# Performance work log

Hardware: AMD Instinct MI355X
Metric: run time of the kernel (lower is better)

The kernel has to match this reference:

```python
import jax, jax.numpy as jnp
import numpy as np

B, Q, K, D = 8, 2048, 2048, 512

def setup_inputs() -> dict:
    key = jax.random.key(0)
    k1, k2, k3, k4, k5 = jax.random.split(key, 5)
    return {
        "query": jax.random.normal(k1, (B, Q, D), dtype=jnp.float32),
        "key": jax.random.normal(k2, (B, K, D), dtype=jnp.float32),
        "value": jax.random.normal(k3, (B, K, D), dtype=jnp.float32),
        "key_mask": jax.random.randint(k4, (B, K), 0, 2, dtype=jnp.int32),
        "W": jax.random.normal(k5, (D, D), dtype=jnp.float32) / np.sqrt(D),
    }

def reference(query, key, value, key_mask, W):
    # bilinear score: s[b,q,k] = query[b,q,:] @ W @ key[b,k,:]
    scale = 1.0 / jnp.sqrt(jnp.asarray(query.shape[-1], query.dtype))
    qW = jnp.einsum('bqd,de->bqe', query, W)          # [B,Q,D]
    scores = jnp.einsum('bqe,bke->bqk', qW, key)      # [B,Q,K]
    scores = jnp.where(key_mask[:, None, :] == 0, jnp.asarray(-1e20, scores.dtype), scores) * scale
    dist = jax.nn.softmax(scores, axis=-1)            # [B,Q,K]
    context = jnp.einsum('bqk,bkd->bqd', dist, value) # [B,Q,D]
    return context, dist
```

## Files before the change

### kernel.cpp

```cpp
#include <hip/hip_runtime.h>
#include <stdint.h>

#define BB 8
#define QQ 2048
#define KK 2048
#define DD 512

typedef _Float16 f16x8 __attribute__((ext_vector_type(8)));
typedef float f32x4 __attribute__((ext_vector_type(4)));

__device__ __forceinline__ unsigned short f2h(float f) {
    union { _Float16 h; unsigned short u; } x;
    x.h = (_Float16)f;
    return x.u;
}
__device__ __forceinline__ float h2f(unsigned short u) {
    union { unsigned short u; _Float16 h; } x;
    x.u = u;
    return (float)x.h;
}

__device__ __forceinline__ void async16(const unsigned short* g, unsigned short* l) {
    __builtin_amdgcn_global_load_lds(
        (const __attribute__((address_space(1))) unsigned int*)g,
        (__attribute__((address_space(3))) unsigned int*)l, 16, 0, 0);
}

__global__ __launch_bounds__(256) void cvt_f32_f16(const float* __restrict__ in,
                                                   unsigned short* __restrict__ out) {
    size_t i = ((size_t)blockIdx.x * 256 + threadIdx.x) * 8;
    float4 a = *(const float4*)(in + i);
    float4 b = *(const float4*)(in + i + 4);
    uint4 u;
    u.x = (unsigned)f2h(a.x) | ((unsigned)f2h(a.y) << 16);
    u.y = (unsigned)f2h(a.z) | ((unsigned)f2h(a.w) << 16);
    u.z = (unsigned)f2h(b.x) | ((unsigned)f2h(b.y) << 16);
    u.w = (unsigned)f2h(b.z) | ((unsigned)f2h(b.w) << 16);
    *(uint4*)(out + i) = u;
}

__global__ __launch_bounds__(256) void transpose_cvt(const float* __restrict__ in,
                                                     unsigned short* __restrict__ out,
                                                     int R, int C, long inB, long outB) {
    __shared__ float t[32][33];
    const float* ip = in + (size_t)blockIdx.z * inB;
    unsigned short* op = out + (size_t)blockIdx.z * outB;
    int x = threadIdx.x & 31, y0 = threadIdx.x >> 5;
    int c0 = blockIdx.x * 32, r0 = blockIdx.y * 32;
#pragma unroll
    for (int i = 0; i < 32; i += 8)
        t[y0 + i][x] = ip[(size_t)(r0 + y0 + i) * C + c0 + x];
    __syncthreads();
#pragma unroll
    for (int i = 0; i < 32; i += 8)
        op[(size_t)(c0 + y0 + i) * R + r0 + x] = f2h(t[x][y0 + i]);
}

template <bool AF32, int OUTM>
__global__ __launch_bounds__(256) void gemm_bt(const void* __restrict__ Aall,
                                               const unsigned short* __restrict__ Ball,
                                               void* __restrict__ Call,
                                               const int* __restrict__ maskAll,
                                               int Kred, int lda, int ldb, int ldc,
                                               long aStride, long bStride, long cStride,
                                               int maskStride, float scale) {
    const int b = blockIdx.z;
    const int m0 = blockIdx.y * 128;
    const int n0 = blockIdx.x * 128;

    __shared__ unsigned short As[128 * 32];
    __shared__ unsigned short Bs[128 * 32];

    const int tid = threadIdx.x;
    const int lane = tid & 63, wave = tid >> 6;
    const int wm = wave >> 1, wn = wave & 1;
    const int lrow = lane & 15, quad = lane >> 4;

    const int ar = tid >> 2, ac = (tid & 3) * 8;
    const int fr = tid >> 3, fc = (tid & 7) * 4;

    const unsigned short* Bb = Ball + (size_t)b * bStride + (size_t)n0 * ldb;
    unsigned short* AsW = As + wave * 512;
    unsigned short* BsW = Bs + wave * 512;

    f32x4 acc[4][4];
#pragma unroll
    for (int mi = 0; mi < 4; mi++)
#pragma unroll
        for (int ni = 0; ni < 4; ni++)
            acc[mi][ni] = (f32x4){0.f, 0.f, 0.f, 0.f};

    for (int kk = 0; kk < Kred; kk += 32) {
        if constexpr (AF32) {
            const float* A = (const float*)Aall + (size_t)b * aStride + (size_t)m0 * lda + kk;
#pragma unroll
            for (int j = 0; j < 4; j++) {
                int row = j * 32 + fr;
                float4 f = *(const float4*)(A + (size_t)row * lda + fc);
                uint2 u;
                u.x = (unsigned)f2h(f.x) | ((unsigned)f2h(f.y) << 16);
                u.y = (unsigned)f2h(f.z) | ((unsigned)f2h(f.w) << 16);
                *(uint2*)&As[row * 32 + fc] = u;
            }
        } else {
            const unsigned short* A =
                (const unsigned short*)Aall + (size_t)b * aStride + (size_t)m0 * lda + kk;
#pragma unroll
            for (int j = 0; j < 2; j++)
                async16(A + (size_t)(j * 64 + ar) * lda + ac, AsW + j * 2048);
        }
        {
            const unsigned short* Bp = Bb + kk;
#pragma unroll
            for (int j = 0; j < 2; j++)
                async16(Bp + (size_t)(j * 64 + ar) * ldb + ac, BsW + j * 2048);
        }
        __syncthreads();

        f16x8 af[4], bfr[4];
#pragma unroll
        for (int i = 0; i < 4; i++)
            af[i] = *(const f16x8*)&As[(wm * 64 + i * 16 + lrow) * 32 + quad * 8];
#pragma unroll
        for (int i = 0; i < 4; i++)
            bfr[i] = *(const f16x8*)&Bs[(wn * 64 + i * 16 + lrow) * 32 + quad * 8];

#pragma unroll
        for (int mi = 0; mi < 4; mi++)
#pragma unroll
            for (int ni = 0; ni < 4; ni++)
                acc[mi][ni] = __builtin_amdgcn_mfma_f32_16x16x32_f16(af[mi], bfr[ni],
                                                                     acc[mi][ni], 0, 0, 0);
        __syncthreads();
    }

#pragma unroll
    for (int mi = 0; mi < 4; mi++) {
#pragma unroll
        for (int ni = 0; ni < 4; ni++) {
            int gm = m0 + wm * 64 + mi * 16 + quad * 4;
            int gn = n0 + wn * 64 + ni * 16 + lrow;
            if constexpr (OUTM == 0) {
                unsigned short* C = (unsigned short*)Call + (size_t)b * cStride;
#pragma unroll
                for (int r = 0; r < 4; r++)
                    C[(size_t)(gm + r) * ldc + gn] = f2h(acc[mi][ni][r]);
            } else if constexpr (OUTM == 1) {
                unsigned short* C = (unsigned short*)Call + (size_t)b * cStride;
                const int* mk = maskAll + (size_t)b * maskStride;
                bool keep = mk[gn] != 0;
#pragma unroll
                for (int r = 0; r < 4; r++)
                    C[(size_t)(gm + r) * ldc + gn] =
                        keep ? f2h(acc[mi][ni][r] * scale) : f2h(-60000.f);
            } else {
                float* C = (float*)Call + (size_t)b * cStride;
#pragma unroll
                for (int r = 0; r < 4; r++)
                    C[(size_t)(gm + r) * ldc + gn] = acc[mi][ni][r];
            }
        }
    }
}

__global__ __launch_bounds__(256) void softmax_rows(unsigned short* __restrict__ sc,
                                                    float* __restrict__ dist) {
    unsigned short* sp = sc + (size_t)blockIdx.x * 2048;
    float* dp = dist + (size_t)blockIdx.x * 2048;
    int tid = threadIdx.x;

    uint4 u = *(uint4*)(sp + tid * 8);
    float x[8];
    x[0] = h2f((unsigned short)(u.x & 0xffff)); x[1] = h2f((unsigned short)(u.x >> 16));
    x[2] = h2f((unsigned short)(u.y & 0xffff)); x[3] = h2f((unsigned short)(u.y >> 16));
    x[4] = h2f((unsigned short)(u.z & 0xffff)); x[5] = h2f((unsigned short)(u.z >> 16));
    x[6] = h2f((unsigned short)(u.w & 0xffff)); x[7] = h2f((unsigned short)(u.w >> 16));

    float m = x[0];
#pragma unroll
    for (int i = 1; i < 8; i++) m = fmaxf(m, x[i]);
#pragma unroll
    for (int off = 32; off > 0; off >>= 1) m = fmaxf(m, __shfl_down(m, off));

    __shared__ float red[8];
    if ((tid & 63) == 0) red[tid >> 6] = m;
    __syncthreads();
    m = fmaxf(fmaxf(red[0], red[1]), fmaxf(red[2], red[3]));

    float s = 0.f;
#pragma unroll
    for (int i = 0; i < 8; i++) { x[i] = __expf(x[i] - m); s += x[i]; }
#pragma unroll
    for (int off = 32; off > 0; off >>= 1) s += __shfl_down(s, off);
    if ((tid & 63) == 0) red[4 + (tid >> 6)] = s;
    __syncthreads();
    float inv = 1.0f / (red[4] + red[5] + red[6] + red[7]);

#pragma unroll
    for (int i = 0; i < 8; i++) x[i] *= inv;

    float4 o0 = {x[0], x[1], x[2], x[3]};
    float4 o1 = {x[4], x[5], x[6], x[7]};
    *(float4*)(dp + tid * 8) = o0;
    *(float4*)(dp + tid * 8 + 4) = o1;

    uint4 v;
    v.x = (unsigned)f2h(x[0]) | ((unsigned)f2h(x[1]) << 16);
    v.y = (unsigned)f2h(x[2]) | ((unsigned)f2h(x[3]) << 16);
    v.z = (unsigned)f2h(x[4]) | ((unsigned)f2h(x[5]) << 16);
    v.w = (unsigned)f2h(x[6]) | ((unsigned)f2h(x[7]) << 16);
    *(uint4*)(sp + tid * 8) = v;
}

extern "C" void kernel_launch(void* const* d_in, const int* in_sizes, int n_in,
                              void* d_out, int out_size, void* d_ws, size_t ws_size,
                              hipStream_t stream) {
    const float* q    = (const float*)d_in[0];
    const float* k    = (const float*)d_in[1];
    const float* v    = (const float*)d_in[2];
    const int*   mask = (const int*)d_in[3];
    const float* W    = (const float*)d_in[4];

    float* ctx  = (float*)d_out;
    float* dist = ctx + (size_t)BB * QQ * DD;

    unsigned short* ws  = (unsigned short*)d_ws;
    unsigned short* Wt  = ws;
    unsigned short* Kh  = Wt + (size_t)DD * DD;
    unsigned short* Vt  = Kh + (size_t)BB * KK * DD;
    unsigned short* qWh = Vt + (size_t)BB * DD * KK;
    unsigned short* Sc  = qWh + (size_t)BB * QQ * DD;

    const float scale = 0.044194173824159216f;

    transpose_cvt<<<dim3(DD / 32, DD / 32, 1), 256, 0, stream>>>(W, Wt, DD, DD, 0, 0);
    cvt_f32_f16<<<dim3((BB * KK * DD / 8) / 256), 256, 0, stream>>>(k, Kh);
    transpose_cvt<<<dim3(DD / 32, KK / 32, BB), 256, 0, stream>>>(
        v, Vt, KK, DD, (long)KK * DD, (long)DD * KK);
    gemm_bt<true, 0><<<dim3(DD / 128, QQ / 128, BB), 256, 0, stream>>>(
        q, Wt, qWh, nullptr, DD, DD, DD, DD,
        (long)QQ * DD, 0, (long)QQ * DD, 0, 0.f);
    gemm_bt<false, 1><<<dim3(KK / 128, QQ / 128, BB), 256, 0, stream>>>(
        qWh, Kh, Sc, mask, DD, DD, DD, KK,
        (long)QQ * DD, (long)KK * DD, (long)QQ * KK, KK, scale);
    softmax_rows<<<dim3(BB * QQ), 256, 0, stream>>>(Sc, dist);
    gemm_bt<false, 2><<<dim3(DD / 128, QQ / 128, BB), 256, 0, stream>>>(
        Sc, Vt, ctx, nullptr, KK, KK, KK, DD,
        (long)QQ * KK, (long)DD * KK, (long)QQ * DD, 0, 0.f);
}
```

Before: 425.1 us.

## Fuse exp and row-sum into score GEMM epilogue, defer softmax normalization

The score GEMM epilogue now writes exp(score*scale) directly, without subtracting a row max, and accumulates per-row sums with shuffles and atomics. The softmax kernel becomes a simple normalize pass, and the context GEMM divides by the row sum in its epilogue instead of reading normalized probabilities. The query is also pre-converted to fp16 so the first GEMM can use async LDS loads. Skipping the max subtraction assumes bounded scores, and exp values stored in fp16 can overflow or lose precision. The extra conversion pass and the atomics add some overhead.

```diff
diff --git a/kernel.cpp b/kernel.cpp
--- a/kernel.cpp
+++ b/kernel.cpp
@@ -56,11 +56,12 @@
         op[(size_t)(c0 + y0 + i) * R + r0 + x] = f2h(t[x][y0 + i]);
 }
 
-template <bool AF32, int OUTM>
-__global__ __launch_bounds__(256) void gemm_bt(const void* __restrict__ Aall,
+template <int OUTM>
+__global__ __launch_bounds__(256) void gemm_bt(const unsigned short* __restrict__ Aall,
                                                const unsigned short* __restrict__ Ball,
                                                void* __restrict__ Call,
                                                const int* __restrict__ maskAll,
+                                               float* __restrict__ sums,
                                                int Kred, int lda, int ldb, int ldc,
                                                long aStride, long bStride, long cStride,
                                                int maskStride, float scale) {
@@ -77,8 +78,8 @@
     const int lrow = lane & 15, quad = lane >> 4;
 
     const int ar = tid >> 2, ac = (tid & 3) * 8;
-    const int fr = tid >> 3, fc = (tid & 7) * 4;
-
+
+    const unsigned short* Ab = Aall + (size_t)b * aStride + (size_t)m0 * lda;
     const unsigned short* Bb = Ball + (size_t)b * bStride + (size_t)n0 * ldb;
     unsigned short* AsW = As + wave * 512;
     unsigned short* BsW = Bs + wave * 512;
@@ -91,30 +92,12 @@
             acc[mi][ni] = (f32x4){0.f, 0.f, 0.f, 0.f};
 
     for (int kk = 0; kk < Kred; kk += 32) {
-        if constexpr (AF32) {
-            const float* A = (const float*)Aall + (size_t)b * aStride + (size_t)m0 * lda + kk;
-#pragma unroll
-            for (int j = 0; j < 4; j++) {
-                int row = j * 32 + fr;
-                float4 f = *(const float4*)(A + (size_t)row * lda + fc);
-                uint2 u;
-                u.x = (unsigned)f2h(f.x) | ((unsigned)f2h(f.y) << 16);
-                u.y = (unsigned)f2h(f.z) | ((unsigned)f2h(f.w) << 16);
-                *(uint2*)&As[row * 32 + fc] = u;
-            }
-        } else {
-            const unsigned short* A =
-                (const unsigned short*)Aall + (size_t)b * aStride + (size_t)m0 * lda + kk;
-#pragma unroll
-            for (int j = 0; j < 2; j++)
-                async16(A + (size_t)(j * 64 + ar) * lda + ac, AsW + j * 2048);
-        }
-        {
-            const unsigned short* Bp = Bb + kk;
-#pragma unroll
-            for (int j = 0; j < 2; j++)
-                async16(Bp + (size_t)(j * 64 + ar) * ldb + ac, BsW + j * 2048);
-        }
+#pragma unroll
+        for (int j = 0; j < 2; j++)
+            async16(Ab + (size_t)(j * 64 + ar) * lda + kk + ac, AsW + j * 2048);
+#pragma unroll
+        for (int j = 0; j < 2; j++)
+            async16(Bb + (size_t)(j * 64 + ar) * ldb + kk + ac, BsW + j * 2048);
         __syncthreads();
 
         f16x8 af[4], bfr[4];
@@ -136,80 +119,77 @@
 
 #pragma unroll
     for (int mi = 0; mi < 4; mi++) {
-#pragma unroll
-        for (int ni = 0; ni < 4; ni++) {
-            int gm = m0 + wm * 64 + mi * 16 + quad * 4;
-            int gn = n0 + wn * 64 + ni * 16 + lrow;
-            if constexpr (OUTM == 0) {
-                unsigned short* C = (unsigned short*)Call + (size_t)b * cStride;
+        const int gm = m0 + wm * 64 + mi * 16 + quad * 4;
+        if constexpr (OUTM == 0) {
+            unsigned short* C = (unsigned short*)Call + (size_t)b * cStride;
+#pragma unroll
+            for (int ni = 0; ni < 4; ni++) {
+                int gn = n0 + wn * 64 + ni * 16 + lrow;
 #pragma unroll
                 for (int r = 0; r < 4; r++)
                     C[(size_t)(gm + r) * ldc + gn] = f2h(acc[mi][ni][r]);
-            } else if constexpr (OUTM == 1) {
-                unsigned short* C = (unsigned short*)Call + (size_t)b * cStride;
-                const int* mk = maskAll + (size_t)b * maskStride;
+            }
+        } else if constexpr (OUTM == 1) {
+            unsigned short* C = (unsigned short*)Call + (size_t)b * cStride;
+            const int* mk = maskAll + (size_t)b * maskStride;
+            float ps[4] = {0.f, 0.f, 0.f, 0.f};
+#pragma unroll
+            for (int ni = 0; ni < 4; ni++) {
+                int gn = n0 + wn * 64 + ni * 16 + lrow;
                 bool keep = mk[gn] != 0;
 #pragma unroll
+                for (int r = 0; r < 4; r++) {
+                    float e = keep ? __expf(acc[mi][ni][r] * scale) : 0.f;
+                    C[(size_t)(gm + r) * ldc + gn] = f2h(e);
+                    ps[r] += e;
+                }
+            }
+#pragma unroll
+            for (int off = 1; off < 16; off <<= 1)
+#pragma unroll
+                for (int r = 0; r < 4; r++) ps[r] += __shfl_xor(ps[r], off);
+            if (lrow == 0) {
+                float* s = sums + (size_t)b * QQ;
+#pragma unroll
+                for (int r = 0; r < 4; r++) atomicAdd(&s[gm + r], ps[r]);
+            }
+        } else {
+            float* C = (float*)Call + (size_t)b * cStride;
+            const float* s = sums + (size_t)b * QQ;
+            float iv[4];
+#pragma unroll
+            for (int r = 0; r < 4; r++) iv[r] = 1.0f / s[gm + r];
+#pragma unroll
+            for (int ni = 0; ni < 4; ni++) {
+                int gn = n0 + wn * 64 + ni * 16 + lrow;
+#pragma unroll
                 for (int r = 0; r < 4; r++)
-                    C[(size_t)(gm + r) * ldc + gn] =
-                        keep ? f2h(acc[mi][ni][r] * scale) : f2h(-60000.f);
-            } else {
-                float* C = (float*)Call + (size_t)b * cStride;
-#pragma unroll
-                for (int r = 0; r < 4; r++)
-                    C[(size_t)(gm + r) * ldc + gn] = acc[mi][ni][r];
+                    C[(size_t)(gm + r) * ldc + gn] = acc[mi][ni][r] * iv[r];
             }
         }
     }
 }
 
-__global__ __launch_bounds__(256) void softmax_rows(unsigned short* __restrict__ sc,
-                                                    float* __restrict__ dist) {
-    unsigned short* sp = sc + (size_t)blockIdx.x * 2048;
+__global__ __launch_bounds__(256) void normalize_rows(const unsigned short* __restrict__ expS,
+                                                      const float* __restrict__ sums,
+                                                      float* __restrict__ dist) {
+    const unsigned short* sp = expS + (size_t)blockIdx.x * 2048;
     float* dp = dist + (size_t)blockIdx.x * 2048;
+    const float inv = 1.0f / sums[blockIdx.x];
     int tid = threadIdx.x;
 
-    uint4 u = *(uint4*)(sp + tid * 8);
-    float x[8];
-    x[0] = h2f((unsigned short)(u.x & 0xffff)); x[1] = h2f((unsigned short)(u.x >> 16));
-    x[2] = h2f((unsigned short)(u.y & 0xffff)); x[3] = h2f((unsigned short)(u.y >> 16));
-    x[4] = h2f((unsigned short)(u.z & 0xffff)); x[5] = h2f((unsigned short)(u.z >> 16));
-    x[6] = h2f((unsigned short)(u.w & 0xffff)); x[7] = h2f((unsigned short)(u.w >> 16));
-
-    float m = x[0];
-#pragma unroll
-    for (int i = 1; i < 8; i++) m = fmaxf(m, x[i]);
-#pragma unroll
-    for (int off = 32; off > 0; off >>= 1) m = fmaxf(m, __shfl_down(m, off));
-
-    __shared__ float red[8];
-    if ((tid & 63) == 0) red[tid >> 6] = m;
-    __syncthreads();
-    m = fmaxf(fmaxf(red[0], red[1]), fmaxf(red[2], red[3]));
-
-    float s = 0.f;
-#pragma unroll
-    for (int i = 0; i < 8; i++) { x[i] = __expf(x[i] - m); s += x[i]; }
-#pragma unroll
-    for (int off = 32; off > 0; off >>= 1) s += __shfl_down(s, off);
-    if ((tid & 63) == 0) red[4 + (tid >> 6)] = s;
-    __syncthreads();
-    float inv = 1.0f / (red[4] + red[5] + red[6] + red[7]);
-
-#pragma unroll
-    for (int i = 0; i < 8; i++) x[i] *= inv;
-
-    float4 o0 = {x[0], x[1], x[2], x[3]};
-    float4 o1 = {x[4], x[5], x[6], x[7]};
+    uint4 u = *(const uint4*)(sp + tid * 8);
+    float4 o0, o1;
+    o0.x = h2f((unsigned short)(u.x & 0xffff)) * inv;
+    o0.y = h2f((unsigned short)(u.x >> 16)) * inv;
+    o0.z = h2f((unsigned short)(u.y & 0xffff)) * inv;
+    o0.w = h2f((unsigned short)(u.y >> 16)) * inv;
+    o1.x = h2f((unsigned short)(u.z & 0xffff)) * inv;
+    o1.y = h2f((unsigned short)(u.z >> 16)) * inv;
+    o1.z = h2f((unsigned short)(u.w & 0xffff)) * inv;
+    o1.w = h2f((unsigned short)(u.w >> 16)) * inv;
     *(float4*)(dp + tid * 8) = o0;
     *(float4*)(dp + tid * 8 + 4) = o1;
-
-    uint4 v;
-    v.x = (unsigned)f2h(x[0]) | ((unsigned)f2h(x[1]) << 16);
-    v.y = (unsigned)f2h(x[2]) | ((unsigned)f2h(x[3]) << 16);
-    v.z = (unsigned)f2h(x[4]) | ((unsigned)f2h(x[5]) << 16);
-    v.w = (unsigned)f2h(x[6]) | ((unsigned)f2h(x[7]) << 16);
-    *(uint4*)(sp + tid * 8) = v;
 }
 
 extern "C" void kernel_launch(void* const* d_in, const int* in_sizes, int n_in,
@@ -226,25 +206,29 @@
 
     unsigned short* ws  = (unsigned short*)d_ws;
     unsigned short* Wt  = ws;
-    unsigned short* Kh  = Wt + (size_t)DD * DD;
+    unsigned short* Qh  = Wt + (size_t)DD * DD;
+    unsigned short* Kh  = Qh + (size_t)BB * QQ * DD;
     unsigned short* Vt  = Kh + (size_t)BB * KK * DD;
     unsigned short* qWh = Vt + (size_t)BB * DD * KK;
     unsigned short* Sc  = qWh + (size_t)BB * QQ * DD;
+    float* sums = (float*)(Sc + (size_t)BB * QQ * KK);
 
     const float scale = 0.044194173824159216f;
 
+    hipMemsetAsync(sums, 0, (size_t)BB * QQ * sizeof(float), stream);
     transpose_cvt<<<dim3(DD / 32, DD / 32, 1), 256, 0, stream>>>(W, Wt, DD, DD, 0, 0);
+    cvt_f32_f16<<<dim3((BB * QQ * DD / 8) / 256), 256, 0, stream>>>(q, Qh);
     cvt_f32_f16<<<dim3((BB * KK * DD / 8) / 256), 256, 0, stream>>>(k, Kh);
     transpose_cvt<<<dim3(DD / 32, KK / 32, BB), 256, 0, stream>>>(
         v, Vt, KK, DD, (long)KK * DD, (long)DD * KK);
-    gemm_bt<true, 0><<<dim3(DD / 128, QQ / 128, BB), 256, 0, stream>>>(
-        q, Wt, qWh, nullptr, DD, DD, DD, DD,
+    gemm_bt<0><<<dim3(DD / 128, QQ / 128, BB), 256, 0, stream>>>(
+        Qh, Wt, qWh, nullptr, nullptr, DD, DD, DD, DD,
         (long)QQ * DD, 0, (long)QQ * DD, 0, 0.f);
-    gemm_bt<false, 1><<<dim3(KK / 128, QQ / 128, BB), 256, 0, stream>>>(
-        qWh, Kh, Sc, mask, DD, DD, DD, KK,
+    gemm_bt<1><<<dim3(KK / 128, QQ / 128, BB), 256, 0, stream>>>(
+        qWh, Kh, Sc, mask, sums, DD, DD, DD, KK,
         (long)QQ * DD, (long)KK * DD, (long)QQ * KK, KK, scale);
-    softmax_rows<<<dim3(BB * QQ), 256, 0, stream>>>(Sc, dist);
-    gemm_bt<false, 2><<<dim3(DD / 128, QQ / 128, BB), 256, 0, stream>>>(
-        Sc, Vt, ctx, nullptr, KK, KK, KK, DD,
+    normalize_rows<<<dim3(BB * QQ), 256, 0, stream>>>(Sc, sums, dist);
+    gemm_bt<2><<<dim3(DD / 128, QQ / 128, BB), 256, 0, stream>>>(
+        Sc, Vt, ctx, nullptr, sums, KK, KK, KK, DD,
         (long)QQ * KK, (long)DD * KK, (long)QQ * DD, 0, 0.f);
 }
```

New measurement: 421.0 us. About the same (-1.0%).
